# Kernel tuning notes

Measured on AMD Instinct MI355X. Metric: run time of the kernel, lower is better.

## Reference

```python
import jax, jax.numpy as jnp
import numpy as np

N_NODES = 100000
N_EDGES = 3200000
IN_DIM, HD_DIM, OUT_DIM = 128, 64, 32


def setup_inputs() -> dict:
    key = jax.random.key(0)
    ks = jax.random.split(key, 8)
    x = jax.random.normal(ks[0], (N_NODES, IN_DIM), dtype=jnp.float32)
    drop_u = jax.random.uniform(ks[1], (N_NODES, IN_DIM), dtype=jnp.float32)
    adj_val = jax.random.uniform(ks[2], (N_EDGES,), dtype=jnp.float32)
    adj_row = jax.random.randint(ks[3], (N_EDGES,), 0, N_NODES, dtype=jnp.int32)
    adj_col = jax.random.randint(ks[4], (N_EDGES,), 0, N_NODES, dtype=jnp.int32)
    W0 = jax.random.normal(ks[5], (IN_DIM, HD_DIM), dtype=jnp.float32) * (1.0 / np.sqrt(IN_DIM))
    b0 = jnp.zeros((HD_DIM,), dtype=jnp.float32)
    W1 = jax.random.normal(ks[6], (HD_DIM, OUT_DIM), dtype=jnp.float32) * (1.0 / np.sqrt(HD_DIM))
    b1 = jnp.zeros((OUT_DIM,), dtype=jnp.float32)
    return {"x": x, "drop_u": drop_u, "adj_val": adj_val, "adj_row": adj_row,
            "adj_col": adj_col, "W0": W0, "b0": b0, "W1": W1, "b1": b1}


def _spmm(val, row, col, h):
    # sparse [N,N] @ dense [N,D]: out[i] = sum_{e: row[e]=i} val[e] * h[col[e]]
    gathered = val[:, None] * h[col]          # [E, D] irregular gather
    return jax.ops.segment_sum(gathered, row, num_segments=N_NODES)


def reference(x, drop_u, adj_val, adj_row, adj_col, W0, b0, W1, b1):
    # dropout p=0.5 (training): keep where u >= 0.5, scale by 1/(1-p)=2
    mask = (drop_u >= 0.5).astype(x.dtype) * 2.0
    h = x * mask
    h = h @ W0 + b0                     # li0: [N, hd]
    h = _spmm(adj_val, adj_row, adj_col, h)
    h = jax.nn.relu(h)
    h = h @ W1 + b1                     # li1: [N, out]
    out = _spmm(adj_val, adj_row, adj_col, h)
    return out
```

## Files before the change

kernel.cpp:

```cpp
#include <hip/hip_runtime.h>

#define NN 100000
#define NE 3200000
#define EB 4096
#define NBP 782
#define BSH 9
#define BRW 512
#define NBK 196

typedef short short8 __attribute__((ext_vector_type(8)));
typedef float f32x4 __attribute__((ext_vector_type(4)));

static __device__ __forceinline__ unsigned short f2bf(float f) {
  union { float f; unsigned int u; } c; c.f = f;
  unsigned int r = c.u + 0x7FFFu + ((c.u >> 16) & 1u);
  return (unsigned short)(r >> 16);
}
static __device__ __forceinline__ float lo16(unsigned int w) {
  union { unsigned int u; float f; } c; c.u = w << 16; return c.f;
}
static __device__ __forceinline__ float hi16(unsigned int w) {
  union { unsigned int u; float f; } c; c.u = w & 0xFFFF0000u; return c.f;
}


__global__ __launch_bounds__(256) void k_phist(const int* __restrict__ row,
                                               int* __restrict__ bcnt) {
  __shared__ int h[NBK];
  int t = threadIdx.x;
  if (t < NBK) h[t] = 0;
  __syncthreads();
  int e0 = blockIdx.x * EB;
  int n = min(EB, NE - e0);
  for (int i = t; i < n; i += 256) atomicAdd(&h[row[e0 + i] >> BSH], 1);
  __syncthreads();
  if (t < NBK && h[t]) atomicAdd(&bcnt[t], h[t]);
}

__global__ __launch_bounds__(256) void k_bscan(const int* __restrict__ bcnt,
                                               int* __restrict__ bbase,
                                               int* __restrict__ bcur) {
  __shared__ int s[256];
  int t = threadIdx.x;
  int v = (t < NBK) ? bcnt[t] : 0;
  s[t] = v;
  __syncthreads();
  for (int off = 1; off < 256; off <<= 1) {
    int a = (t >= off) ? s[t - off] : 0;
    __syncthreads();
    s[t] += a;
    __syncthreads();
  }
  int ex = s[t] - v;
  if (t < NBK) { bbase[t] = ex; bcur[t] = ex; }
  if (t == NBK - 1) bbase[NBK] = ex + v;
}

__global__ __launch_bounds__(256) void k_part(const int* __restrict__ row,
                                              const int* __restrict__ col,
                                              const float* __restrict__ val,
                                              int* __restrict__ bcur,
                                              uint2* __restrict__ tmp) {
  __shared__ uint2 stage[EB];
  __shared__ int dst[EB];
  __shared__ int h[NBK];
  __shared__ int bex[NBK];
  __shared__ int win[NBK];
  __shared__ int c2[NBK];
  __shared__ int sc[256];
  int t = threadIdx.x;
  int e0 = blockIdx.x * EB;
  int n = min(EB, NE - e0);
  if (t < NBK) { h[t] = 0; c2[t] = 0; }
  __syncthreads();
  for (int i = t; i < n; i += 256) atomicAdd(&h[row[e0 + i] >> BSH], 1);
  __syncthreads();
  int v = (t < NBK) ? h[t] : 0;
  sc[t] = v;
  __syncthreads();
  for (int off = 1; off < 256; off <<= 1) {
    int a = (t >= off) ? sc[t - off] : 0;
    __syncthreads();
    sc[t] += a;
    __syncthreads();
  }
  int ex = sc[t] - v;
  if (t < NBK) {
    bex[t] = ex;
    win[t] = v ? atomicAdd(&bcur[t], v) : 0;
  }
  __syncthreads();
  for (int i = t; i < n; i += 256) {
    int e = e0 + i;
    int r = row[e];
    unsigned int c = (unsigned int)col[e];
    float vv = val[e];
    int b = r >> BSH;
    int rank = atomicAdd(&c2[b], 1);
    int s_ = bex[b] + rank;
    uint2 w;
    w.x = __float_as_uint(vv);
    w.y = ((unsigned int)(r & (BRW - 1)) << 17) | c;
    stage[s_] = w;
    dst[s_] = win[b] + rank;
  }
  __syncthreads();
  for (int i = t; i < n; i += 256) tmp[dst[i]] = stage[i];
}

__global__ __launch_bounds__(512) void k_bsort(const int* __restrict__ bbase,
                                               const uint2* __restrict__ tmp,
                                               uint2* __restrict__ vc,
                                               int* __restrict__ rp) {
  __shared__ int cnt[BRW];
  __shared__ int pre[BRW];
  __shared__ int c2[BRW];
  int t = threadIdx.x;
  int b = blockIdx.x;
  int s0 = bbase[b], s1 = bbase[b + 1];
  int n = s1 - s0;
  cnt[t] = 0; c2[t] = 0;
  __syncthreads();
  for (int i = t; i < n; i += 512) atomicAdd(&cnt[tmp[s0 + i].y >> 17], 1);
  __syncthreads();
  int v = cnt[t];
  pre[t] = v;
  __syncthreads();
  for (int off = 1; off < 512; off <<= 1) {
    int a = (t >= off) ? pre[t - off] : 0;
    __syncthreads();
    pre[t] += a;
    __syncthreads();
  }
  int ex = pre[t] - v;
  int r = (b << BSH) + t;
  if (r < NN) rp[r] = s0 + ex;
  if (b == NBK - 1 && t == 0) rp[NN] = NE;
  pre[t] = ex;
  __syncthreads();
  for (int i = t; i < n; i += 512) {
    uint2 w = tmp[s0 + i];
    int rl = (int)(w.y >> 17);
    int rank = atomicAdd(&c2[rl], 1);
    int pos = s0 + pre[rl] + rank;
    uint2 o;
    o.x = w.x;
    o.y = w.y & 0x1FFFFu;
    vc[pos] = o;
  }
}


__global__ __launch_bounds__(256) void k_wcvt(const float* __restrict__ W0,
                                              unsigned short* __restrict__ W0bT) {
  int t = threadIdx.x;
#pragma unroll
  for (int i = 0; i < 32; ++i) {
    int idx = t + i * 256;
    int n = idx >> 7, k = idx & 127;
    W0bT[idx] = f2bf(W0[(size_t)k * 64 + n]);
  }
}

__global__ __launch_bounds__(256) void k_gemm0(const float* __restrict__ x,
                                               const float* __restrict__ u,
                                               const unsigned short* __restrict__ W0bT,
                                               const float* __restrict__ b0,
                                               unsigned short* __restrict__ h0b) {
  __shared__ unsigned short xs[64][136];
  int t = threadIdx.x;
  int r0 = blockIdx.x * 64;
#pragma unroll
  for (int i = 0; i < 8; ++i) {
    int f4 = t + i * 256;
    int row = f4 >> 5;
    int off = f4 & 31;
    int r = r0 + row;
    float4 m = make_float4(0.f, 0.f, 0.f, 0.f);
    if (r < NN) {
      float4 xv = ((const float4*)(x + (size_t)r * 128))[off];
      float4 uv = ((const float4*)(u + (size_t)r * 128))[off];
      m.x = (uv.x >= 0.5f) ? xv.x : 0.f;
      m.y = (uv.y >= 0.5f) ? xv.y : 0.f;
      m.z = (uv.z >= 0.5f) ? xv.z : 0.f;
      m.w = (uv.w >= 0.5f) ? xv.w : 0.f;
    }
    uint2 pk;
    pk.x = (unsigned int)f2bf(m.x) | ((unsigned int)f2bf(m.y) << 16);
    pk.y = (unsigned int)f2bf(m.z) | ((unsigned int)f2bf(m.w) << 16);
    *(uint2*)&xs[row][off * 4] = pk;
  }
  __syncthreads();

  int lane = t & 63;
  int wv = __builtin_amdgcn_readfirstlane(t >> 6);
  int arow = wv * 16 + (lane & 15);
  int kgrp = lane >> 4;
  int ncol = lane & 15;

  short8 afrag[4];
#pragma unroll
  for (int kb = 0; kb < 4; ++kb)
    afrag[kb] = *(const short8*)&xs[arow][kgrp * 8 + kb * 32];

  short8 bfrag[4][4];
#pragma unroll
  for (int kb = 0; kb < 4; ++kb)
#pragma unroll
    for (int nb = 0; nb < 4; ++nb)
      bfrag[kb][nb] = *(const short8*)&W0bT[(size_t)(nb * 16 + ncol) * 128 +
                                            kgrp * 8 + kb * 32];

  f32x4 acc[4];
#pragma unroll
  for (int nb = 0; nb < 4; ++nb) acc[nb] = (f32x4)(0.f);
#pragma unroll
  for (int kb = 0; kb < 4; ++kb)
#pragma unroll
    for (int nb = 0; nb < 4; ++nb)
      acc[nb] = __builtin_amdgcn_mfma_f32_16x16x32_bf16(afrag[kb], bfrag[kb][nb],
                                                        acc[nb], 0, 0, 0);

#pragma unroll
  for (int nb = 0; nb < 4; ++nb) {
    int c = nb * 16 + ncol;
    float bias = b0[c];
#pragma unroll
    for (int reg = 0; reg < 4; ++reg) {
      int rr = r0 + wv * 16 + kgrp * 4 + reg;
      if (rr < NN) h0b[(size_t)rr * 64 + c] = f2bf(2.f * acc[nb][reg] + bias);
    }
  }
}


__global__ __launch_bounds__(256) void k_gemm1(const unsigned short* __restrict__ s1b,
                                               const float* __restrict__ W1,
                                               const float* __restrict__ b1,
                                               unsigned short* __restrict__ h1b) {
  __shared__ float ss[128][65];
  int t = threadIdx.x;
  int r0 = blockIdx.x * 128;
#pragma unroll
  for (int i = 0; i < 4; ++i) {
    int q = t + i * 256;
    int row = q >> 3;
    int off = q & 7;
    int r = r0 + row;
    float* dp = &ss[row][off * 8];
    if (r < NN) {
      uint4 w = ((const uint4*)(s1b + (size_t)r * 64))[off];
      unsigned int ws[4] = {w.x, w.y, w.z, w.w};
#pragma unroll
      for (int j = 0; j < 4; ++j) {
        dp[2 * j] = lo16(ws[j]);
        dp[2 * j + 1] = hi16(ws[j]);
      }
    } else {
#pragma unroll
      for (int j = 0; j < 8; ++j) dp[j] = 0.f;
    }
  }
  __syncthreads();

  int lane = t & 63;
  int wv = __builtin_amdgcn_readfirstlane(t >> 6);
  int rloc = (wv >> 1) * 64 + lane;
  int dblk = wv & 1;
  int r = r0 + rloc;
  const float* Wd = W1 + dblk * 16;
  float acc[16];
#pragma unroll
  for (int d = 0; d < 16; ++d) acc[d] = 0.f;
#pragma unroll 1
  for (int kc = 0; kc < 4; ++kc) {
    float sm[16];
#pragma unroll
    for (int k = 0; k < 16; ++k) sm[k] = ss[rloc][kc * 16 + k];
#pragma unroll
    for (int k = 0; k < 16; ++k) {
      const float* wrow = Wd + (size_t)(kc * 16 + k) * 32;
#pragma unroll
      for (int d = 0; d < 16; ++d) acc[d] = fmaf(sm[k], wrow[d], acc[d]);
    }
  }
  if (r >= NN) return;
  unsigned int* o32 = (unsigned int*)(h1b + (size_t)r * 32 + dblk * 16);
  const float* bd = b1 + dblk * 16;
#pragma unroll
  for (int d = 0; d < 8; ++d) {
    float a = acc[2 * d] + bd[2 * d];
    float b = acc[2 * d + 1] + bd[2 * d + 1];
    o32[d] = (unsigned int)f2bf(a) | ((unsigned int)f2bf(b) << 16);
  }
}


__global__ __launch_bounds__(256) void k_spmm1(const int* __restrict__ rp,
                                               const uint2* __restrict__ vc,
                                               const uint2* __restrict__ h0v,
                                               uint2* __restrict__ s1v) {
  int wid = (blockIdx.x * 256 + threadIdx.x) >> 6;
  int lane = threadIdx.x & 63;
  if (wid >= NN) return;
  int qw = lane >> 4;
  int d = lane & 15;
  int j0 = rp[wid], j1 = rp[wid + 1];
  float a0 = 0.f, a1 = 0.f, a2 = 0.f, a3 = 0.f;
  int j = j0 + qw;
  uint2 e0, e1, e2, e3;
  bool have = (j + 12 < j1);
  if (have) { e0 = vc[j]; e1 = vc[j + 4]; e2 = vc[j + 8]; e3 = vc[j + 12]; }
  while (have) {
    uint2 g0 = h0v[(size_t)e0.y * 16 + d];
    uint2 g1 = h0v[(size_t)e1.y * 16 + d];
    uint2 g2 = h0v[(size_t)e2.y * 16 + d];
    uint2 g3 = h0v[(size_t)e3.y * 16 + d];
    float v0 = __uint_as_float(e0.x), v1 = __uint_as_float(e1.x);
    float v2 = __uint_as_float(e2.x), v3 = __uint_as_float(e3.x);
    int jn = j + 16;
    bool hn = (jn + 12 < j1);
    if (hn) { e0 = vc[jn]; e1 = vc[jn + 4]; e2 = vc[jn + 8]; e3 = vc[jn + 12]; }
    a0 = fmaf(v0, lo16(g0.x), a0); a1 = fmaf(v0, hi16(g0.x), a1);
    a2 = fmaf(v0, lo16(g0.y), a2); a3 = fmaf(v0, hi16(g0.y), a3);
    a0 = fmaf(v1, lo16(g1.x), a0); a1 = fmaf(v1, hi16(g1.x), a1);
    a2 = fmaf(v1, lo16(g1.y), a2); a3 = fmaf(v1, hi16(g1.y), a3);
    a0 = fmaf(v2, lo16(g2.x), a0); a1 = fmaf(v2, hi16(g2.x), a1);
    a2 = fmaf(v2, lo16(g2.y), a2); a3 = fmaf(v2, hi16(g2.y), a3);
    a0 = fmaf(v3, lo16(g3.x), a0); a1 = fmaf(v3, hi16(g3.x), a1);
    a2 = fmaf(v3, lo16(g3.y), a2); a3 = fmaf(v3, hi16(g3.y), a3);
    j = jn; have = hn;
  }
  for (; j < j1; j += 4) {
    uint2 e = vc[j];
    uint2 g = h0v[(size_t)e.y * 16 + d];
    float v = __uint_as_float(e.x);
    a0 = fmaf(v, lo16(g.x), a0); a1 = fmaf(v, hi16(g.x), a1);
    a2 = fmaf(v, lo16(g.y), a2); a3 = fmaf(v, hi16(g.y), a3);
  }
  a0 += __shfl_xor(a0, 16); a0 += __shfl_xor(a0, 32);
  a1 += __shfl_xor(a1, 16); a1 += __shfl_xor(a1, 32);
  a2 += __shfl_xor(a2, 16); a2 += __shfl_xor(a2, 32);
  a3 += __shfl_xor(a3, 16); a3 += __shfl_xor(a3, 32);
  if (qw == 0) {
    uint2 pk;
    pk.x = (unsigned int)f2bf(fmaxf(a0, 0.f)) | ((unsigned int)f2bf(fmaxf(a1, 0.f)) << 16);
    pk.y = (unsigned int)f2bf(fmaxf(a2, 0.f)) | ((unsigned int)f2bf(fmaxf(a3, 0.f)) << 16);
    s1v[(size_t)wid * 16 + d] = pk;
  }
}

__global__ __launch_bounds__(256) void k_spmm2(const int* __restrict__ rp,
                                               const uint2* __restrict__ vc,
                                               const uint2* __restrict__ h1v,
                                               float* __restrict__ out) {
  int wid = (blockIdx.x * 256 + threadIdx.x) >> 6;
  int lane = threadIdx.x & 63;
  if (wid >= NN) return;
  int slot = lane >> 3;
  int d = lane & 7;
  int j0 = rp[wid], j1 = rp[wid + 1];
  float a0 = 0.f, a1 = 0.f, a2 = 0.f, a3 = 0.f;
  int j = j0 + slot;
  uint2 e0, e1;
  bool have = (j + 8 < j1);
  if (have) { e0 = vc[j]; e1 = vc[j + 8]; }
  while (have) {
    uint2 g0 = h1v[(size_t)e0.y * 8 + d];
    uint2 g1 = h1v[(size_t)e1.y * 8 + d];
    float v0 = __uint_as_float(e0.x), v1 = __uint_as_float(e1.x);
    int jn = j + 16;
    bool hn = (jn + 8 < j1);
    if (hn) { e0 = vc[jn]; e1 = vc[jn + 8]; }
    a0 = fmaf(v0, lo16(g0.x), a0); a1 = fmaf(v0, hi16(g0.x), a1);
    a2 = fmaf(v0, lo16(g0.y), a2); a3 = fmaf(v0, hi16(g0.y), a3);
    a0 = fmaf(v1, lo16(g1.x), a0); a1 = fmaf(v1, hi16(g1.x), a1);
    a2 = fmaf(v1, lo16(g1.y), a2); a3 = fmaf(v1, hi16(g1.y), a3);
    j = jn; have = hn;
  }
  for (; j < j1; j += 8) {
    uint2 e = vc[j];
    uint2 g = h1v[(size_t)e.y * 8 + d];
    float v = __uint_as_float(e.x);
    a0 = fmaf(v, lo16(g.x), a0); a1 = fmaf(v, hi16(g.x), a1);
    a2 = fmaf(v, lo16(g.y), a2); a3 = fmaf(v, hi16(g.y), a3);
  }
  a0 += __shfl_xor(a0, 8); a0 += __shfl_xor(a0, 16); a0 += __shfl_xor(a0, 32);
  a1 += __shfl_xor(a1, 8); a1 += __shfl_xor(a1, 16); a1 += __shfl_xor(a1, 32);
  a2 += __shfl_xor(a2, 8); a2 += __shfl_xor(a2, 16); a2 += __shfl_xor(a2, 32);
  a3 += __shfl_xor(a3, 8); a3 += __shfl_xor(a3, 16); a3 += __shfl_xor(a3, 32);
  if (slot == 0) {
    ((float4*)(out + (size_t)wid * 32))[d] = make_float4(a0, a1, a2, a3);
  }
}


extern "C" void kernel_launch(void* const* d_in, const int* in_sizes, int n_in,
                              void* d_out, int out_size, void* d_ws, size_t ws_size,
                              hipStream_t stream) {
  const float* x   = (const float*)d_in[0];
  const float* u   = (const float*)d_in[1];
  const float* val = (const float*)d_in[2];
  const int* row   = (const int*)d_in[3];
  const int* col   = (const int*)d_in[4];
  const float* W0  = (const float*)d_in[5];
  const float* b0  = (const float*)d_in[6];
  const float* W1  = (const float*)d_in[7];
  const float* b1  = (const float*)d_in[8];
  float* out = (float*)d_out;

  char* p = (char*)d_ws;
  auto take = [&](size_t bytes) {
    char* q = p;
    p += (bytes + 255) & ~(size_t)255;
    return q;
  };
  uint2* tmp = (uint2*)take((size_t)NE * 8);
  uint2* vc  = (uint2*)take((size_t)NE * 8);
  unsigned short* s1b = (unsigned short*)take((size_t)NN * 64 * 2);
  int* rp    = (int*)take((size_t)(NN + 1) * 4);
  int* bcnt  = (int*)take((size_t)NBK * 4);
  int* bbase = (int*)take((size_t)(NBK + 1) * 4);
  int* bcur  = (int*)take((size_t)NBK * 4);
  unsigned short* w0bt = (unsigned short*)take((size_t)64 * 128 * 2);
  unsigned short* h0b = (unsigned short*)tmp;
  unsigned short* h1b = (unsigned short*)((char*)tmp + (size_t)NN * 64 * 2);

  hipMemsetAsync(bcnt, 0, (size_t)NBK * 4, stream);
  k_phist<<<NBP, 256, 0, stream>>>(row, bcnt);
  k_bscan<<<1, 256, 0, stream>>>(bcnt, bbase, bcur);
  k_part<<<NBP, 256, 0, stream>>>(row, col, val, bcur, tmp);
  k_bsort<<<NBK, 512, 0, stream>>>(bbase, tmp, vc, rp);

  k_wcvt<<<1, 256, 0, stream>>>(W0, w0bt);
  k_gemm0<<<(NN + 63) / 64, 256, 0, stream>>>(x, u, w0bt, b0, h0b);
  k_spmm1<<<(NN + 3) / 4, 256, 0, stream>>>(rp, vc, (const uint2*)h0b,
                                            (uint2*)s1b);
  k_gemm1<<<(NN + 127) / 128, 256, 0, stream>>>(s1b, W1, b1, h1b);
  k_spmm2<<<(NN + 3) / 4, 256, 0, stream>>>(rp, vc, (const uint2*)h1b, out);
}
```

Measured before the change: 260.5 us.

## Use bf16 MFMA for second GEMM and widen partition/sort blocks

```diff
diff --git a/kernel.cpp b/kernel.cpp
--- a/kernel.cpp
+++ b/kernel.cpp
@@ -56,7 +56,7 @@
   if (t == NBK - 1) bbase[NBK] = ex + v;
 }
 
-__global__ __launch_bounds__(256) void k_part(const int* __restrict__ row,
+__global__ __launch_bounds__(512) void k_part(const int* __restrict__ row,
                                               const int* __restrict__ col,
                                               const float* __restrict__ val,
                                               int* __restrict__ bcur,
@@ -67,18 +67,18 @@
   __shared__ int bex[NBK];
   __shared__ int win[NBK];
   __shared__ int c2[NBK];
-  __shared__ int sc[256];
+  __shared__ int sc[512];
   int t = threadIdx.x;
   int e0 = blockIdx.x * EB;
   int n = min(EB, NE - e0);
   if (t < NBK) { h[t] = 0; c2[t] = 0; }
   __syncthreads();
-  for (int i = t; i < n; i += 256) atomicAdd(&h[row[e0 + i] >> BSH], 1);
+  for (int i = t; i < n; i += 512) atomicAdd(&h[row[e0 + i] >> BSH], 1);
   __syncthreads();
   int v = (t < NBK) ? h[t] : 0;
   sc[t] = v;
   __syncthreads();
-  for (int off = 1; off < 256; off <<= 1) {
+  for (int off = 1; off < 512; off <<= 1) {
     int a = (t >= off) ? sc[t - off] : 0;
     __syncthreads();
     sc[t] += a;
@@ -90,7 +90,7 @@
     win[t] = v ? atomicAdd(&bcur[t], v) : 0;
   }
   __syncthreads();
-  for (int i = t; i < n; i += 256) {
+  for (int i = t; i < n; i += 512) {
     int e = e0 + i;
     int r = row[e];
     unsigned int c = (unsigned int)col[e];
@@ -105,13 +105,13 @@
     dst[s_] = win[b] + rank;
   }
   __syncthreads();
-  for (int i = t; i < n; i += 256) tmp[dst[i]] = stage[i];
-}
-
-__global__ __launch_bounds__(512) void k_bsort(const int* __restrict__ bbase,
-                                               const uint2* __restrict__ tmp,
-                                               uint2* __restrict__ vc,
-                                               int* __restrict__ rp) {
+  for (int i = t; i < n; i += 512) tmp[dst[i]] = stage[i];
+}
+
+__global__ __launch_bounds__(1024) void k_bsort(const int* __restrict__ bbase,
+                                                const uint2* __restrict__ tmp,
+                                                uint2* __restrict__ vc,
+                                                int* __restrict__ rp) {
   __shared__ int cnt[BRW];
   __shared__ int pre[BRW];
   __shared__ int c2[BRW];
@@ -119,26 +119,28 @@
   int b = blockIdx.x;
   int s0 = bbase[b], s1 = bbase[b + 1];
   int n = s1 - s0;
-  cnt[t] = 0; c2[t] = 0;
-  __syncthreads();
-  for (int i = t; i < n; i += 512) atomicAdd(&cnt[tmp[s0 + i].y >> 17], 1);
-  __syncthreads();
-  int v = cnt[t];
-  pre[t] = v;
-  __syncthreads();
-  for (int off = 1; off < 512; off <<= 1) {
-    int a = (t >= off) ? pre[t - off] : 0;
-    __syncthreads();
-    pre[t] += a;
-    __syncthreads();
-  }
-  int ex = pre[t] - v;
-  int r = (b << BSH) + t;
-  if (r < NN) rp[r] = s0 + ex;
+  if (t < BRW) { cnt[t] = 0; c2[t] = 0; }
+  __syncthreads();
+  for (int i = t; i < n; i += 1024) atomicAdd(&cnt[tmp[s0 + i].y >> 17], 1);
+  __syncthreads();
+  int v = (t < BRW) ? cnt[t] : 0;
+  if (t < BRW) pre[t] = v;
+  __syncthreads();
+  for (int off = 1; off < BRW; off <<= 1) {
+    int a = (t >= off && t < BRW) ? pre[t - off] : 0;
+    __syncthreads();
+    if (t < BRW) pre[t] += a;
+    __syncthreads();
+  }
+  if (t < BRW) {
+    int ex = pre[t] - v;
+    int r = (b << BSH) + t;
+    if (r < NN) rp[r] = s0 + ex;
+    pre[t] = ex;
+  }
   if (b == NBK - 1 && t == 0) rp[NN] = NE;
-  pre[t] = ex;
-  __syncthreads();
-  for (int i = t; i < n; i += 512) {
+  __syncthreads();
+  for (int i = t; i < n; i += 1024) {
     uint2 w = tmp[s0 + i];
     int rl = (int)(w.y >> 17);
     int rank = atomicAdd(&c2[rl], 1);
@@ -150,17 +152,21 @@
   }
 }
 
-
 __global__ __launch_bounds__(256) void k_wcvt(const float* __restrict__ W0,
-                                              unsigned short* __restrict__ W0bT) {
-  int t = threadIdx.x;
-#pragma unroll
-  for (int i = 0; i < 32; ++i) {
-    int idx = t + i * 256;
+                                              unsigned short* __restrict__ W0bT,
+                                              const float* __restrict__ W1,
+                                              unsigned short* __restrict__ W1bT) {
+  int idx = blockIdx.x * 256 + threadIdx.x;
+  if (idx < 8192) {
     int n = idx >> 7, k = idx & 127;
     W0bT[idx] = f2bf(W0[(size_t)k * 64 + n]);
-  }
-}
+  } else if (idx < 8192 + 2048) {
+    int i2 = idx - 8192;
+    int n = i2 >> 6, k = i2 & 63;
+    W1bT[i2] = f2bf(W1[(size_t)k * 32 + n]);
+  }
+}
+
 
 __global__ __launch_bounds__(256) void k_gemm0(const float* __restrict__ x,
                                                const float* __restrict__ u,
@@ -235,63 +241,62 @@
 
 
 __global__ __launch_bounds__(256) void k_gemm1(const unsigned short* __restrict__ s1b,
-                                               const float* __restrict__ W1,
+                                               const unsigned short* __restrict__ W1bT,
                                                const float* __restrict__ b1,
                                                unsigned short* __restrict__ h1b) {
-  __shared__ float ss[128][65];
-  int t = threadIdx.x;
-  int r0 = blockIdx.x * 128;
-#pragma unroll
-  for (int i = 0; i < 4; ++i) {
+  __shared__ unsigned short ss[64][72];
+  int t = threadIdx.x;
+  int r0 = blockIdx.x * 64;
+#pragma unroll
+  for (int i = 0; i < 2; ++i) {
     int q = t + i * 256;
     int row = q >> 3;
     int off = q & 7;
     int r = r0 + row;
-    float* dp = &ss[row][off * 8];
-    if (r < NN) {
-      uint4 w = ((const uint4*)(s1b + (size_t)r * 64))[off];
-      unsigned int ws[4] = {w.x, w.y, w.z, w.w};
-#pragma unroll
-      for (int j = 0; j < 4; ++j) {
-        dp[2 * j] = lo16(ws[j]);
-        dp[2 * j + 1] = hi16(ws[j]);
-      }
-    } else {
-#pragma unroll
-      for (int j = 0; j < 8; ++j) dp[j] = 0.f;
-    }
+    uint4 w = make_uint4(0u, 0u, 0u, 0u);
+    if (r < NN) w = ((const uint4*)(s1b + (size_t)r * 64))[off];
+    *(uint4*)&ss[row][off * 8] = w;
   }
   __syncthreads();
 
   int lane = t & 63;
   int wv = __builtin_amdgcn_readfirstlane(t >> 6);
-  int rloc = (wv >> 1) * 64 + lane;
-  int dblk = wv & 1;
-  int r = r0 + rloc;
-  const float* Wd = W1 + dblk * 16;
-  float acc[16];
-#pragma unroll
-  for (int d = 0; d < 16; ++d) acc[d] = 0.f;
-#pragma unroll 1
-  for (int kc = 0; kc < 4; ++kc) {
-    float sm[16];
-#pragma unroll
-    for (int k = 0; k < 16; ++k) sm[k] = ss[rloc][kc * 16 + k];
-#pragma unroll
-    for (int k = 0; k < 16; ++k) {
-      const float* wrow = Wd + (size_t)(kc * 16 + k) * 32;
-#pragma unroll
-      for (int d = 0; d < 16; ++d) acc[d] = fmaf(sm[k], wrow[d], acc[d]);
+  int arow = wv * 16 + (lane & 15);
+  int kgrp = lane >> 4;
+  int ncol = lane & 15;
+
+  short8 afrag[2];
+#pragma unroll
+  for (int kb = 0; kb < 2; ++kb)
+    afrag[kb] = *(const short8*)&ss[arow][kgrp * 8 + kb * 32];
+
+  short8 bfrag[2][2];
+#pragma unroll
+  for (int kb = 0; kb < 2; ++kb)
+#pragma unroll
+    for (int nb = 0; nb < 2; ++nb)
+      bfrag[kb][nb] = *(const short8*)&W1bT[(size_t)(nb * 16 + ncol) * 64 +
+                                            kgrp * 8 + kb * 32];
+
+  f32x4 acc[2];
+#pragma unroll
+  for (int nb = 0; nb < 2; ++nb) acc[nb] = (f32x4)(0.f);
+#pragma unroll
+  for (int kb = 0; kb < 2; ++kb)
+#pragma unroll
+    for (int nb = 0; nb < 2; ++nb)
+      acc[nb] = __builtin_amdgcn_mfma_f32_16x16x32_bf16(afrag[kb], bfrag[kb][nb],
+                                                        acc[nb], 0, 0, 0);
+
+#pragma unroll
+  for (int nb = 0; nb < 2; ++nb) {
+    int c = nb * 16 + ncol;
+    float bias = b1[c];
+#pragma unroll
+    for (int reg = 0; reg < 4; ++reg) {
+      int rr = r0 + wv * 16 + kgrp * 4 + reg;
+      if (rr < NN) h1b[(size_t)rr * 32 + c] = f2bf(acc[nb][reg] + bias);
     }
-  }
-  if (r >= NN) return;
-  unsigned int* o32 = (unsigned int*)(h1b + (size_t)r * 32 + dblk * 16);
-  const float* bd = b1 + dblk * 16;
-#pragma unroll
-  for (int d = 0; d < 8; ++d) {
-    float a = acc[2 * d] + bd[2 * d];
-    float b = acc[2 * d + 1] + bd[2 * d + 1];
-    o32[d] = (unsigned int)f2bf(a) | ((unsigned int)f2bf(b) << 16);
   }
 }
 
@@ -423,19 +428,20 @@
   int* bbase = (int*)take((size_t)(NBK + 1) * 4);
   int* bcur  = (int*)take((size_t)NBK * 4);
   unsigned short* w0bt = (unsigned short*)take((size_t)64 * 128 * 2);
+  unsigned short* w1bt = (unsigned short*)take((size_t)32 * 64 * 2);
   unsigned short* h0b = (unsigned short*)tmp;
   unsigned short* h1b = (unsigned short*)((char*)tmp + (size_t)NN * 64 * 2);
 
   hipMemsetAsync(bcnt, 0, (size_t)NBK * 4, stream);
   k_phist<<<NBP, 256, 0, stream>>>(row, bcnt);
   k_bscan<<<1, 256, 0, stream>>>(bcnt, bbase, bcur);
-  k_part<<<NBP, 256, 0, stream>>>(row, col, val, bcur, tmp);
-  k_bsort<<<NBK, 512, 0, stream>>>(bbase, tmp, vc, rp);
-
-  k_wcvt<<<1, 256, 0, stream>>>(W0, w0bt);
+  k_part<<<NBP, 512, 0, stream>>>(row, col, val, bcur, tmp);
+  k_bsort<<<NBK, 1024, 0, stream>>>(bbase, tmp, vc, rp);
+
+  k_wcvt<<<40, 256, 0, stream>>>(W0, w0bt, W1, w1bt);
   k_gemm0<<<(NN + 63) / 64, 256, 0, stream>>>(x, u, w0bt, b0, h0b);
   k_spmm1<<<(NN + 3) / 4, 256, 0, stream>>>(rp, vc, (const uint2*)h0b,
                                             (uint2*)s1b);
-  k_gemm1<<<(NN + 127) / 128, 256, 0, stream>>>(s1b, W1, b1, h1b);
+  k_gemm1<<<(NN + 63) / 64, 256, 0, stream>>>(s1b, w1bt, b1, h1b);
   k_spmm2<<<(NN + 3) / 4, 256, 0, stream>>>(rp, vc, (const uint2*)h1b, out);
 }
```

Result: faster. 239.9 us (-7.9%).
